# Kernel optimization log

Hardware: AMD Instinct MI355X
Metric: run time of the kernel (lower is better)

## Reference

```python
import jax, jax.numpy as jnp
import numpy as np

NUM_EXPERTS = 8
HIDDEN = 1024
INTER = 1024
TOKENS = 2048
TOPK = 2


def setup_inputs() -> dict:
    key = jax.random.key(0)
    ks = jax.random.split(key, 7)
    hidden_states = jax.random.normal(ks[0], (TOKENS, HIDDEN), dtype=jnp.float32)
    router_weights = jax.random.uniform(ks[1], (TOKENS, TOPK), dtype=jnp.float32)
    selected_experts = jax.random.randint(ks[2], (TOKENS, TOPK), 0, NUM_EXPERTS, dtype=jnp.int32)
    token_per_expert = jax.random.randint(ks[3], (NUM_EXPERTS,), 0, 512, dtype=jnp.int32)
    # torch Linear weight layout is [out, in]; chunked along out-dim into E experts.
    # gate/up: [E, INTER, HIDDEN]; down: [E, HIDDEN, INTER]
    scale_h = 1.0 / np.sqrt(HIDDEN)
    scale_i = 1.0 / np.sqrt(INTER)
    gate_w = jax.random.normal(ks[4], (NUM_EXPERTS, INTER, HIDDEN), dtype=jnp.float32) * scale_h
    up_w = jax.random.normal(ks[5], (NUM_EXPERTS, INTER, HIDDEN), dtype=jnp.float32) * scale_h
    down_w = jax.random.normal(ks[6], (NUM_EXPERTS, HIDDEN, INTER), dtype=jnp.float32) * scale_i
    return {
        "hidden_states": hidden_states,
        "router_weights": router_weights,
        "selected_experts": selected_experts,
        "token_per_expert": token_per_expert,
        "gate_w": gate_w,
        "up_w": up_w,
        "down_w": down_w,
    }


def reference(hidden_states, router_weights, selected_experts, token_per_expert, gate_w, up_w, down_w):
    # Math equivalent of permute -> grouped GEMM (gate/up SwiGLU, down) -> unpermute+weighted combine.
    # Each (token, k) pair is routed to expert selected_experts[t,k] and scaled by router_weights[t,k]
    # (cast to fp32 as in the original), then summed over k.
    # Grouped GEMM out = x @ W_e^T; we evaluate every expert densely over all tokens and
    # combine with a one-hot routing matrix (clean, fully vectorized reference).
    x = hidden_states  # [T, H]
    g = jnp.einsum('th,eih->eti', x, gate_w)          # [E, T, I]
    u = jnp.einsum('th,eih->eti', x, up_w)            # [E, T, I]
    h = jax.nn.silu(g) * u                            # [E, T, I]
    out_e = jnp.einsum('eti,ehi->eth', h, down_w)     # [E, T, H]
    # combine[t, e] = sum_k router_weights[t, k] * 1[selected_experts[t, k] == e]
    onehot = jax.nn.one_hot(selected_experts, NUM_EXPERTS, dtype=jnp.float32)  # [T, K, E]
    combine = jnp.einsum('tk,tke->te', router_weights.astype(jnp.float32), onehot)  # [T, E]
    y = jnp.einsum('te,eth->th', combine, out_e)      # [T, H]
    return y
```

## Files before the change

### kernel.cpp

```cpp
#include <hip/hip_runtime.h>
#include <hip/hip_bf16.h>

#define HID   1024
#define NEXP  8
#define NPAIR 4096
#define BMPAD 128
#define PERM_MAX (NPAIR + NEXP * BMPAD)
#define MT_MAX (PERM_MAX / 128)

typedef unsigned short u16;
typedef __attribute__((ext_vector_type(8))) short bf16x8;
typedef __attribute__((ext_vector_type(4))) float f32x4;
typedef __attribute__((ext_vector_type(4))) unsigned short us4;
typedef __attribute__((ext_vector_type(4))) unsigned int u32x4;

static __device__ __forceinline__ u16 f2bf(float f) {
  union { float f; unsigned u; } v; v.f = f;
  unsigned u = v.u;
  unsigned r = (u + 0x7fffu + ((u >> 16) & 1u)) >> 16;
  return (u16)r;
}

static __device__ __forceinline__ unsigned pk2(float a, float b) {
  __hip_bfloat162 h = __float22bfloat162_rn(make_float2(a, b));
  union { __hip_bfloat162 h; unsigned u; } c; c.h = h; return c.u;
}

static __device__ __forceinline__ void gload16(const void* g, void* l) {
  __builtin_amdgcn_global_load_lds(
      (const __attribute__((address_space(1))) unsigned int*)g,
      (__attribute__((address_space(3))) unsigned int*)l, 16, 0, 0);
}

static __device__ __forceinline__ f32x4 mfma_bf16(bf16x8 a, bf16x8 b, f32x4 c) {
  return __builtin_amdgcn_mfma_f32_16x16x32_bf16(a, b, c, 0, 0, 0);
}

__global__ __launch_bounds__(256) void k_prep(const float* __restrict__ x,
                                              u16* __restrict__ xb,
                                              float* __restrict__ out) {
  int i = blockIdx.x * 256 + threadIdx.x;
  int base = i * 8;
  f32x4 v0 = *(const f32x4*)(x + base);
  f32x4 v1 = *(const f32x4*)(x + base + 4);
  us4 a = { f2bf(v0[0]), f2bf(v0[1]), f2bf(v0[2]), f2bf(v0[3]) };
  us4 b = { f2bf(v1[0]), f2bf(v1[1]), f2bf(v1[2]), f2bf(v1[3]) };
  *(us4*)(xb + base)     = a;
  *(us4*)(xb + base + 4) = b;
  f32x4 z = {0.f, 0.f, 0.f, 0.f};
  *(f32x4*)(out + base)     = z;
  *(f32x4*)(out + base + 4) = z;
}

__global__ __launch_bounds__(256) void k_route(const int* __restrict__ sel,
                                               int* __restrict__ hdr,
                                               int* __restrict__ perm) {
  __shared__ int cnt[NEXP];
  __shared__ int cur[NEXP];
  int tid = threadIdx.x;
  if (tid < NEXP) cnt[tid] = 0;
  __syncthreads();
  for (int p = tid; p < NPAIR; p += 256) atomicAdd(&cnt[sel[p]], 1);
  __syncthreads();
  if (tid == 0) {
    int acc = 0;
    for (int e = 0; e < NEXP; e++) {
      hdr[e] = acc;
      cur[e] = acc;
      acc += (cnt[e] + 127) & ~127;
    }
    hdr[NEXP] = acc;
  }
  __syncthreads();
  for (int i = tid; i < PERM_MAX; i += 256) perm[i] = -1;
  __syncthreads();
  for (int p = tid; p < NPAIR; p += 256) {
    int e = sel[p];
    int slot = atomicAdd(&cur[e], 1);
    perm[slot] = p;
  }
}

__global__ __launch_bounds__(256) void k_gateup(const u16* __restrict__ xb,
                                                const float* __restrict__ gw,
                                                const float* __restrict__ uw,
                                                const int* __restrict__ hdr,
                                                const int* __restrict__ perm,
                                                u16* __restrict__ hbuf) {
  __shared__ __align__(16) u16 lA[2][128 * 64];
  __shared__ __align__(16) u16 lBg[2][64 * 64];
  __shared__ __align__(16) u16 lBu[2][64 * 64];

  const int tid = threadIdx.x, lane = tid & 63, wv = tid >> 6;
  const int n0 = blockIdx.x * 64, m0 = blockIdx.y * 128;
  if (m0 >= hdr[NEXP]) return;
  int e = 0;
  #pragma unroll
  for (int k = 1; k < NEXP; k++) if (m0 >= hdr[k]) e = k;

  const u16* srcA[4]; int dstAo[4];
  #pragma unroll
  for (int j = 0; j < 4; j++) {
    int rt = wv * 32 + j * 8 + (lane >> 3);
    int p = perm[m0 + rt];
    int tok = (p < 0) ? 0 : (p >> 1);
    int sw = (lane & 7) ^ (rt & 7);
    srcA[j] = xb + (size_t)tok * HID + sw * 8;
    dstAo[j] = (wv * 32 + j * 8) * 64;
  }
  const int br = wv * 16 + (lane >> 2);
  const int cb = (lane & 3) * 16;
  const size_t eb = (size_t)e * (1 << 20);
  const float* pG = gw + eb + (size_t)(n0 + br) * HID + cb;
  const float* pU = uw + eb + (size_t)(n0 + br) * HID + cb;
  const int bws0 = br * 64 + ((((lane & 3) * 2 + 0) ^ (br & 7)) * 8);
  const int bws1 = br * 64 + ((((lane & 3) * 2 + 1) ^ (br & 7)) * 8);

  const int wm = wv >> 1, wn = wv & 1;
  const int fr = lane & 15, fq = lane >> 4;

  f32x4 vg[4], vu[4];
  f32x4 accg[4][2], accu[4][2];
  #pragma unroll
  for (int a = 0; a < 4; a++)
    #pragma unroll
    for (int b = 0; b < 2; b++) {
      accg[a][b] = (f32x4){0.f, 0.f, 0.f, 0.f};
      accu[a][b] = (f32x4){0.f, 0.f, 0.f, 0.f};
    }

#define GU_ISSUE(B, K0) { const int k0_ = (K0);                                   \
    _Pragma("unroll") for (int j = 0; j < 4; j++)                                 \
      gload16(srcA[j] + k0_, &lA[B][dstAo[j]]);                                   \
    _Pragma("unroll") for (int i = 0; i < 4; i++) {                               \
      vg[i] = *(const f32x4*)(pG + k0_ + i * 4);                                  \
      vu[i] = *(const f32x4*)(pU + k0_ + i * 4);                                  \
    } }

#define GU_CVTW(B) {                                                              \
    u32x4 w0 = { pk2(vg[0][0], vg[0][1]), pk2(vg[0][2], vg[0][3]),                \
                 pk2(vg[1][0], vg[1][1]), pk2(vg[1][2], vg[1][3]) };              \
    *(u32x4*)&lBg[B][bws0] = w0;                                                  \
    u32x4 w1 = { pk2(vg[2][0], vg[2][1]), pk2(vg[2][2], vg[2][3]),                \
                 pk2(vg[3][0], vg[3][1]), pk2(vg[3][2], vg[3][3]) };              \
    *(u32x4*)&lBg[B][bws1] = w1;                                                  \
    u32x4 w2 = { pk2(vu[0][0], vu[0][1]), pk2(vu[0][2], vu[0][3]),                \
                 pk2(vu[1][0], vu[1][1]), pk2(vu[1][2], vu[1][3]) };              \
    *(u32x4*)&lBu[B][bws0] = w2;                                                  \
    u32x4 w3 = { pk2(vu[2][0], vu[2][1]), pk2(vu[2][2], vu[2][3]),                \
                 pk2(vu[3][0], vu[3][1]), pk2(vu[3][2], vu[3][3]) };              \
    *(u32x4*)&lBu[B][bws1] = w3; }

#define GU_COMP(B) {                                                              \
    _Pragma("unroll") for (int kk2 = 0; kk2 < 2; kk2++) {                         \
      bf16x8 af[4], bg[2], bu[2];                                                 \
      _Pragma("unroll") for (int m2 = 0; m2 < 4; m2++) {                          \
        int r = wm * 64 + m2 * 16 + fr, q = kk2 * 4 + fq;                         \
        af[m2] = *(const bf16x8*)&lA[B][r * 64 + (q ^ (r & 7)) * 8];              \
      }                                                                           \
      _Pragma("unroll") for (int n2 = 0; n2 < 2; n2++) {                          \
        int r = wn * 32 + n2 * 16 + fr, q = kk2 * 4 + fq;                         \
        bg[n2] = *(const bf16x8*)&lBg[B][r * 64 + (q ^ (r & 7)) * 8];             \
        bu[n2] = *(const bf16x8*)&lBu[B][r * 64 + (q ^ (r & 7)) * 8];             \
      }                                                                           \
      _Pragma("unroll") for (int m2 = 0; m2 < 4; m2++)                            \
        _Pragma("unroll") for (int n2 = 0; n2 < 2; n2++) {                        \
          accg[m2][n2] = mfma_bf16(af[m2], bg[n2], accg[m2][n2]);                 \
          accu[m2][n2] = mfma_bf16(af[m2], bu[n2], accu[m2][n2]);                 \
        }                                                                         \
    } }

  GU_ISSUE(0, 0);
  GU_CVTW(0);
  __syncthreads();
  for (int kk = 0; kk < 16; kk += 2) {
    GU_ISSUE(1, (kk + 1) * 64);
    GU_COMP(0);
    GU_CVTW(1);
    __syncthreads();
    if (kk + 2 < 16) { GU_ISSUE(0, (kk + 2) * 64); }
    GU_COMP(1);
    if (kk + 2 < 16) { GU_CVTW(0); }
    __syncthreads();
  }
#undef GU_ISSUE
#undef GU_CVTW
#undef GU_COMP

  #pragma unroll
  for (int m2 = 0; m2 < 4; m2++)
    #pragma unroll
    for (int n2 = 0; n2 < 2; n2++)
      #pragma unroll
      for (int q = 0; q < 4; q++) {
        int row = m0 + wm * 64 + m2 * 16 + fq * 4 + q;
        int col = n0 + wn * 32 + n2 * 16 + fr;
        float g = accg[m2][n2][q];
        float u = accu[m2][n2][q];
        float h = (g / (1.0f + __expf(-g))) * u;
        hbuf[(size_t)row * HID + col] = f2bf(h);
      }
}

__global__ __launch_bounds__(256) void k_down(const u16* __restrict__ hbuf,
                                              const float* __restrict__ dw,
                                              const int* __restrict__ hdr,
                                              const int* __restrict__ perm,
                                              const float* __restrict__ rw,
                                              float* __restrict__ out) {
  __shared__ __align__(16) u16 lA[2][128 * 64];
  __shared__ __align__(16) u16 lB[2][64 * 64];

  const int tid = threadIdx.x, lane = tid & 63, wv = tid >> 6;
  const int n0 = blockIdx.x * 64, m0 = blockIdx.y * 128;
  if (m0 >= hdr[NEXP]) return;
  int e = 0;
  #pragma unroll
  for (int k = 1; k < NEXP; k++) if (m0 >= hdr[k]) e = k;

  const u16* srcA[4]; int dstAo[4];
  #pragma unroll
  for (int j = 0; j < 4; j++) {
    int rt = wv * 32 + j * 8 + (lane >> 3);
    int sw = (lane & 7) ^ (rt & 7);
    srcA[j] = hbuf + (size_t)(m0 + rt) * HID + sw * 8;
    dstAo[j] = (wv * 32 + j * 8) * 64;
  }
  const int br = wv * 16 + (lane >> 2);
  const int cb = (lane & 3) * 16;
  const size_t eb = (size_t)e * (1 << 20);
  const float* pB = dw + eb + (size_t)(n0 + br) * HID + cb;
  const int bws0 = br * 64 + ((((lane & 3) * 2 + 0) ^ (br & 7)) * 8);
  const int bws1 = br * 64 + ((((lane & 3) * 2 + 1) ^ (br & 7)) * 8);

  const int wm = wv >> 1, wn = wv & 1;
  const int fr = lane & 15, fq = lane >> 4;

  f32x4 vb[4];
  f32x4 acc[4][2];
  #pragma unroll
  for (int a = 0; a < 4; a++)
    #pragma unroll
    for (int b = 0; b < 2; b++) acc[a][b] = (f32x4){0.f, 0.f, 0.f, 0.f};

#define DN_ISSUE(B, K0) { const int k0_ = (K0);                                   \
    _Pragma("unroll") for (int j = 0; j < 4; j++)                                 \
      gload16(srcA[j] + k0_, &lA[B][dstAo[j]]);                                   \
    _Pragma("unroll") for (int i = 0; i < 4; i++)                                 \
      vb[i] = *(const f32x4*)(pB + k0_ + i * 4); }

#define DN_CVTW(B) {                                                              \
    u32x4 w0 = { pk2(vb[0][0], vb[0][1]), pk2(vb[0][2], vb[0][3]),                \
                 pk2(vb[1][0], vb[1][1]), pk2(vb[1][2], vb[1][3]) };              \
    *(u32x4*)&lB[B][bws0] = w0;                                                   \
    u32x4 w1 = { pk2(vb[2][0], vb[2][1]), pk2(vb[2][2], vb[2][3]),                \
                 pk2(vb[3][0], vb[3][1]), pk2(vb[3][2], vb[3][3]) };              \
    *(u32x4*)&lB[B][bws1] = w1; }

#define DN_COMP(B) {                                                              \
    _Pragma("unroll") for (int kk2 = 0; kk2 < 2; kk2++) {                         \
      bf16x8 af[4], bf[2];                                                        \
      _Pragma("unroll") for (int m2 = 0; m2 < 4; m2++) {                          \
        int r = wm * 64 + m2 * 16 + fr, q = kk2 * 4 + fq;                         \
        af[m2] = *(const bf16x8*)&lA[B][r * 64 + (q ^ (r & 7)) * 8];              \
      }                                                                           \
      _Pragma("unroll") for (int n2 = 0; n2 < 2; n2++) {                          \
        int r = wn * 32 + n2 * 16 + fr, q = kk2 * 4 + fq;                         \
        bf[n2] = *(const bf16x8*)&lB[B][r * 64 + (q ^ (r & 7)) * 8];              \
      }                                                                           \
      _Pragma("unroll") for (int m2 = 0; m2 < 4; m2++)                            \
        _Pragma("unroll") for (int n2 = 0; n2 < 2; n2++)                          \
          acc[m2][n2] = mfma_bf16(af[m2], bf[n2], acc[m2][n2]);                   \
    } }

  DN_ISSUE(0, 0);
  DN_CVTW(0);
  __syncthreads();
  for (int kk = 0; kk < 16; kk += 2) {
    DN_ISSUE(1, (kk + 1) * 64);
    DN_COMP(0);
    DN_CVTW(1);
    __syncthreads();
    if (kk + 2 < 16) { DN_ISSUE(0, (kk + 2) * 64); }
    DN_COMP(1);
    if (kk + 2 < 16) { DN_CVTW(0); }
    __syncthreads();
  }
#undef DN_ISSUE
#undef DN_CVTW
#undef DN_COMP

  #pragma unroll
  for (int m2 = 0; m2 < 4; m2++)
    #pragma unroll
    for (int q = 0; q < 4; q++) {
      int row = m0 + wm * 64 + m2 * 16 + fq * 4 + q;
      int p = perm[row];
      if (p < 0) continue;
      int t = p >> 1;
      float w = rw[p];
      #pragma unroll
      for (int n2 = 0; n2 < 2; n2++) {
        int col = n0 + wn * 32 + n2 * 16 + fr;
        atomicAdd(&out[(size_t)t * HID + col], acc[m2][n2][q] * w);
      }
    }
}

extern "C" void kernel_launch(void* const* d_in, const int* in_sizes, int n_in,
                              void* d_out, int out_size, void* d_ws, size_t ws_size,
                              hipStream_t stream) {
  const float* x   = (const float*)d_in[0];
  const float* rw  = (const float*)d_in[1];
  const int*   sel = (const int*)d_in[2];
  const float* gw  = (const float*)d_in[4];
  const float* uw  = (const float*)d_in[5];
  const float* dw  = (const float*)d_in[6];
  float* out = (float*)d_out;

  char* ws = (char*)d_ws;
  int*  hdr  = (int*)ws;
  int*  perm = (int*)(ws + 1024);
  u16*  xb   = (u16*)(ws + (1 << 16));
  u16*  hbuf = xb + (2 << 20);

  k_prep <<<dim3(1024), dim3(256), 0, stream>>>(x, xb, out);
  k_route<<<dim3(1),    dim3(256), 0, stream>>>(sel, hdr, perm);
  k_gateup<<<dim3(16, MT_MAX), dim3(256), 0, stream>>>(xb, gw, uw, hdr, perm, hbuf);
  k_down  <<<dim3(16, MT_MAX), dim3(256), 0, stream>>>(hbuf, dw, hdr, perm, rw, out);
}
```

Measured before the change: 115.3 us.

## Load expert weights straight into MFMA registers, drop LDS staging for B

Each wave now loads its own fp32 weight rows from global memory and converts them to bf16 MFMA B fragments in registers, so the B tile no longer goes through LDS. Every wave covers all 128 token rows against its own 16 or 32 output columns. The down kernel widens its N tile to 128, which halves its grid, and both kernels use a 1D grid with a remapped tile order plus a launch-bounds occupancy hint. This removes the LDS writes and reads and the barrier pressure for weights, at the cost of more registers and less coalesced per-lane global loads.

```diff
diff --git a/kernel.cpp b/kernel.cpp
--- a/kernel.cpp
+++ b/kernel.cpp
@@ -12,7 +12,6 @@
 typedef __attribute__((ext_vector_type(8))) short bf16x8;
 typedef __attribute__((ext_vector_type(4))) float f32x4;
 typedef __attribute__((ext_vector_type(4))) unsigned short us4;
-typedef __attribute__((ext_vector_type(4))) unsigned int u32x4;
 
 static __device__ __forceinline__ u16 f2bf(float f) {
   union { float f; unsigned u; } v; v.f = f;
@@ -24,6 +23,13 @@
 static __device__ __forceinline__ unsigned pk2(float a, float b) {
   __hip_bfloat162 h = __float22bfloat162_rn(make_float2(a, b));
   union { __hip_bfloat162 h; unsigned u; } c; c.h = h; return c.u;
+}
+
+static __device__ __forceinline__ bf16x8 cvt8(f32x4 a, f32x4 b) {
+  union { unsigned u[4]; bf16x8 v; } r;
+  r.u[0] = pk2(a[0], a[1]); r.u[1] = pk2(a[2], a[3]);
+  r.u[2] = pk2(b[0], b[1]); r.u[3] = pk2(b[2], b[3]);
+  return r.v;
 }
 
 static __device__ __forceinline__ void gload16(const void* g, void* l) {
@@ -81,18 +87,20 @@
   }
 }
 
-__global__ __launch_bounds__(256) void k_gateup(const u16* __restrict__ xb,
-                                                const float* __restrict__ gw,
-                                                const float* __restrict__ uw,
-                                                const int* __restrict__ hdr,
-                                                const int* __restrict__ perm,
-                                                u16* __restrict__ hbuf) {
+__global__ __launch_bounds__(256, 3) void k_gateup(const u16* __restrict__ xb,
+                                                   const float* __restrict__ gw,
+                                                   const float* __restrict__ uw,
+                                                   const int* __restrict__ hdr,
+                                                   const int* __restrict__ perm,
+                                                   u16* __restrict__ hbuf) {
   __shared__ __align__(16) u16 lA[2][128 * 64];
-  __shared__ __align__(16) u16 lBg[2][64 * 64];
-  __shared__ __align__(16) u16 lBu[2][64 * 64];
 
   const int tid = threadIdx.x, lane = tid & 63, wv = tid >> 6;
-  const int n0 = blockIdx.x * 64, m0 = blockIdx.y * 128;
+  const int wgid = blockIdx.x;
+  const int slot = wgid >> 3;
+  const int nt = ((slot & 1) << 3) | (wgid & 7);
+  const int mt = slot >> 1;
+  const int n0 = nt * 64, m0 = mt * 128;
   if (m0 >= hdr[NEXP]) return;
   int e = 0;
   #pragma unroll
@@ -108,111 +116,94 @@
     srcA[j] = xb + (size_t)tok * HID + sw * 8;
     dstAo[j] = (wv * 32 + j * 8) * 64;
   }
-  const int br = wv * 16 + (lane >> 2);
-  const int cb = (lane & 3) * 16;
+
+  const int fr = lane & 15, fq = lane >> 4;
   const size_t eb = (size_t)e * (1 << 20);
-  const float* pG = gw + eb + (size_t)(n0 + br) * HID + cb;
-  const float* pU = uw + eb + (size_t)(n0 + br) * HID + cb;
-  const int bws0 = br * 64 + ((((lane & 3) * 2 + 0) ^ (br & 7)) * 8);
-  const int bws1 = br * 64 + ((((lane & 3) * 2 + 1) ^ (br & 7)) * 8);
-
-  const int wm = wv >> 1, wn = wv & 1;
-  const int fr = lane & 15, fq = lane >> 4;
-
-  f32x4 vg[4], vu[4];
-  f32x4 accg[4][2], accu[4][2];
-  #pragma unroll
-  for (int a = 0; a < 4; a++)
+  const int brow = n0 + wv * 16 + fr;
+  const float* pG = gw + eb + (size_t)brow * HID + fq * 8;
+  const float* pU = uw + eb + (size_t)brow * HID + fq * 8;
+
+  f32x4 ng[2][2], nu[2][2];
+  bf16x8 fg[2], fu[2];
+  f32x4 ag[8], au[8];
+  #pragma unroll
+  for (int i = 0; i < 8; i++) {
+    ag[i] = (f32x4){0.f, 0.f, 0.f, 0.f};
+    au[i] = (f32x4){0.f, 0.f, 0.f, 0.f};
+  }
+
+#define GU_GLA(B, K0) {                                                        \
+    _Pragma("unroll") for (int j = 0; j < 4; j++)                              \
+      gload16(srcA[j] + (K0), &lA[B][dstAo[j]]); }
+
+#define GU_LOADB(K0) {                                                         \
+    _Pragma("unroll") for (int kk2 = 0; kk2 < 2; kk2++) {                      \
+      ng[kk2][0] = *(const f32x4*)(pG + (K0) + kk2 * 32);                      \
+      ng[kk2][1] = *(const f32x4*)(pG + (K0) + kk2 * 32 + 4);                  \
+      nu[kk2][0] = *(const f32x4*)(pU + (K0) + kk2 * 32);                      \
+      nu[kk2][1] = *(const f32x4*)(pU + (K0) + kk2 * 32 + 4);                  \
+    } }
+
+#define GU_CVTB() {                                                            \
+    fg[0] = cvt8(ng[0][0], ng[0][1]); fg[1] = cvt8(ng[1][0], ng[1][1]);        \
+    fu[0] = cvt8(nu[0][0], nu[0][1]); fu[1] = cvt8(nu[1][0], nu[1][1]); }
+
+#define GU_COMP(B) {                                                           \
+    _Pragma("unroll") for (int kk2 = 0; kk2 < 2; kk2++) {                      \
+      _Pragma("unroll") for (int m2 = 0; m2 < 8; m2++) {                       \
+        int r = m2 * 16 + fr, q = kk2 * 4 + fq;                                \
+        bf16x8 af = *(const bf16x8*)&lA[B][r * 64 + (q ^ (r & 7)) * 8];        \
+        ag[m2] = mfma_bf16(af, fg[kk2], ag[m2]);                               \
+        au[m2] = mfma_bf16(af, fu[kk2], au[m2]);                               \
+      }                                                                        \
+    } }
+
+  GU_GLA(0, 0);
+  GU_LOADB(0);
+  __syncthreads();
+  GU_CVTB();
+  for (int kk = 0; kk < 16; kk += 2) {
+    GU_GLA(1, (kk + 1) * 64);
+    GU_LOADB((kk + 1) * 64);
+    GU_COMP(0);
+    __syncthreads();
+    GU_CVTB();
+    if (kk + 2 < 16) { GU_GLA(0, (kk + 2) * 64); GU_LOADB((kk + 2) * 64); }
+    GU_COMP(1);
+    __syncthreads();
+    if (kk + 2 < 16) GU_CVTB();
+  }
+#undef GU_GLA
+#undef GU_LOADB
+#undef GU_CVTB
+#undef GU_COMP
+
+  #pragma unroll
+  for (int m2 = 0; m2 < 8; m2++)
     #pragma unroll
-    for (int b = 0; b < 2; b++) {
-      accg[a][b] = (f32x4){0.f, 0.f, 0.f, 0.f};
-      accu[a][b] = (f32x4){0.f, 0.f, 0.f, 0.f};
+    for (int q = 0; q < 4; q++) {
+      int row = m0 + m2 * 16 + fq * 4 + q;
+      int col = n0 + wv * 16 + fr;
+      float g = ag[m2][q];
+      float u = au[m2][q];
+      float h = (g / (1.0f + __expf(-g))) * u;
+      hbuf[(size_t)row * HID + col] = f2bf(h);
     }
-
-#define GU_ISSUE(B, K0) { const int k0_ = (K0);                                   \
-    _Pragma("unroll") for (int j = 0; j < 4; j++)                                 \
-      gload16(srcA[j] + k0_, &lA[B][dstAo[j]]);                                   \
-    _Pragma("unroll") for (int i = 0; i < 4; i++) {                               \
-      vg[i] = *(const f32x4*)(pG + k0_ + i * 4);                                  \
-      vu[i] = *(const f32x4*)(pU + k0_ + i * 4);                                  \
-    } }
-
-#define GU_CVTW(B) {                                                              \
-    u32x4 w0 = { pk2(vg[0][0], vg[0][1]), pk2(vg[0][2], vg[0][3]),                \
-                 pk2(vg[1][0], vg[1][1]), pk2(vg[1][2], vg[1][3]) };              \
-    *(u32x4*)&lBg[B][bws0] = w0;                                                  \
-    u32x4 w1 = { pk2(vg[2][0], vg[2][1]), pk2(vg[2][2], vg[2][3]),                \
-                 pk2(vg[3][0], vg[3][1]), pk2(vg[3][2], vg[3][3]) };              \
-    *(u32x4*)&lBg[B][bws1] = w1;                                                  \
-    u32x4 w2 = { pk2(vu[0][0], vu[0][1]), pk2(vu[0][2], vu[0][3]),                \
-                 pk2(vu[1][0], vu[1][1]), pk2(vu[1][2], vu[1][3]) };              \
-    *(u32x4*)&lBu[B][bws0] = w2;                                                  \
-    u32x4 w3 = { pk2(vu[2][0], vu[2][1]), pk2(vu[2][2], vu[2][3]),                \
-                 pk2(vu[3][0], vu[3][1]), pk2(vu[3][2], vu[3][3]) };              \
-    *(u32x4*)&lBu[B][bws1] = w3; }
-
-#define GU_COMP(B) {                                                              \
-    _Pragma("unroll") for (int kk2 = 0; kk2 < 2; kk2++) {                         \
-      bf16x8 af[4], bg[2], bu[2];                                                 \
-      _Pragma("unroll") for (int m2 = 0; m2 < 4; m2++) {                          \
-        int r = wm * 64 + m2 * 16 + fr, q = kk2 * 4 + fq;                         \
-        af[m2] = *(const bf16x8*)&lA[B][r * 64 + (q ^ (r & 7)) * 8];              \
-      }                                                                           \
-      _Pragma("unroll") for (int n2 = 0; n2 < 2; n2++) {                          \
-        int r = wn * 32 + n2 * 16 + fr, q = kk2 * 4 + fq;                         \
-        bg[n2] = *(const bf16x8*)&lBg[B][r * 64 + (q ^ (r & 7)) * 8];             \
-        bu[n2] = *(const bf16x8*)&lBu[B][r * 64 + (q ^ (r & 7)) * 8];             \
-      }                                                                           \
-      _Pragma("unroll") for (int m2 = 0; m2 < 4; m2++)                            \
-        _Pragma("unroll") for (int n2 = 0; n2 < 2; n2++) {                        \
-          accg[m2][n2] = mfma_bf16(af[m2], bg[n2], accg[m2][n2]);                 \
-          accu[m2][n2] = mfma_bf16(af[m2], bu[n2], accu[m2][n2]);                 \
-        }                                                                         \
-    } }
-
-  GU_ISSUE(0, 0);
-  GU_CVTW(0);
-  __syncthreads();
-  for (int kk = 0; kk < 16; kk += 2) {
-    GU_ISSUE(1, (kk + 1) * 64);
-    GU_COMP(0);
-    GU_CVTW(1);
-    __syncthreads();
-    if (kk + 2 < 16) { GU_ISSUE(0, (kk + 2) * 64); }
-    GU_COMP(1);
-    if (kk + 2 < 16) { GU_CVTW(0); }
-    __syncthreads();
-  }
-#undef GU_ISSUE
-#undef GU_CVTW
-#undef GU_COMP
-
-  #pragma unroll
-  for (int m2 = 0; m2 < 4; m2++)
-    #pragma unroll
-    for (int n2 = 0; n2 < 2; n2++)
-      #pragma unroll
-      for (int q = 0; q < 4; q++) {
-        int row = m0 + wm * 64 + m2 * 16 + fq * 4 + q;
-        int col = n0 + wn * 32 + n2 * 16 + fr;
-        float g = accg[m2][n2][q];
-        float u = accu[m2][n2][q];
-        float h = (g / (1.0f + __expf(-g))) * u;
-        hbuf[(size_t)row * HID + col] = f2bf(h);
-      }
-}
-
-__global__ __launch_bounds__(256) void k_down(const u16* __restrict__ hbuf,
-                                              const float* __restrict__ dw,
-                                              const int* __restrict__ hdr,
-                                              const int* __restrict__ perm,
-                                              const float* __restrict__ rw,
-                                              float* __restrict__ out) {
+}
+
+__global__ __launch_bounds__(256, 3) void k_down(const u16* __restrict__ hbuf,
+                                                 const float* __restrict__ dw,
+                                                 const int* __restrict__ hdr,
+                                                 const int* __restrict__ perm,
+                                                 const float* __restrict__ rw,
+                                                 float* __restrict__ out) {
   __shared__ __align__(16) u16 lA[2][128 * 64];
-  __shared__ __align__(16) u16 lB[2][64 * 64];
 
   const int tid = threadIdx.x, lane = tid & 63, wv = tid >> 6;
-  const int n0 = blockIdx.x * 64, m0 = blockIdx.y * 128;
+  const int wgid = blockIdx.x;
+  const int nt = wgid & 7;
+  const int mt = wgid >> 3;
+  const int n0 = nt * 128, m0 = mt * 128;
   if (m0 >= hdr[NEXP]) return;
   int e = 0;
   #pragma unroll
@@ -226,82 +217,82 @@
     srcA[j] = hbuf + (size_t)(m0 + rt) * HID + sw * 8;
     dstAo[j] = (wv * 32 + j * 8) * 64;
   }
-  const int br = wv * 16 + (lane >> 2);
-  const int cb = (lane & 3) * 16;
+
+  const int fr = lane & 15, fq = lane >> 4;
   const size_t eb = (size_t)e * (1 << 20);
-  const float* pB = dw + eb + (size_t)(n0 + br) * HID + cb;
-  const int bws0 = br * 64 + ((((lane & 3) * 2 + 0) ^ (br & 7)) * 8);
-  const int bws1 = br * 64 + ((((lane & 3) * 2 + 1) ^ (br & 7)) * 8);
-
-  const int wm = wv >> 1, wn = wv & 1;
-  const int fr = lane & 15, fq = lane >> 4;
-
-  f32x4 vb[4];
-  f32x4 acc[4][2];
-  #pragma unroll
-  for (int a = 0; a < 4; a++)
+  const float* pB[2];
+  #pragma unroll
+  for (int n2 = 0; n2 < 2; n2++) {
+    int brow = n0 + wv * 32 + n2 * 16 + fr;
+    pB[n2] = dw + eb + (size_t)brow * HID + fq * 8;
+  }
+
+  f32x4 nb[2][2][2];
+  bf16x8 fb[2][2];
+  f32x4 acc[8][2];
+  #pragma unroll
+  for (int i = 0; i < 8; i++)
     #pragma unroll
-    for (int b = 0; b < 2; b++) acc[a][b] = (f32x4){0.f, 0.f, 0.f, 0.f};
-
-#define DN_ISSUE(B, K0) { const int k0_ = (K0);                                   \
-    _Pragma("unroll") for (int j = 0; j < 4; j++)                                 \
-      gload16(srcA[j] + k0_, &lA[B][dstAo[j]]);                                   \
-    _Pragma("unroll") for (int i = 0; i < 4; i++)                                 \
-      vb[i] = *(const f32x4*)(pB + k0_ + i * 4); }
-
-#define DN_CVTW(B) {                                                              \
-    u32x4 w0 = { pk2(vb[0][0], vb[0][1]), pk2(vb[0][2], vb[0][3]),                \
-                 pk2(vb[1][0], vb[1][1]), pk2(vb[1][2], vb[1][3]) };              \
-    *(u32x4*)&lB[B][bws0] = w0;                                                   \
-    u32x4 w1 = { pk2(vb[2][0], vb[2][1]), pk2(vb[2][2], vb[2][3]),                \
-                 pk2(vb[3][0], vb[3][1]), pk2(vb[3][2], vb[3][3]) };              \
-    *(u32x4*)&lB[B][bws1] = w1; }
-
-#define DN_COMP(B) {                                                              \
-    _Pragma("unroll") for (int kk2 = 0; kk2 < 2; kk2++) {                         \
-      bf16x8 af[4], bf[2];                                                        \
-      _Pragma("unroll") for (int m2 = 0; m2 < 4; m2++) {                          \
-        int r = wm * 64 + m2 * 16 + fr, q = kk2 * 4 + fq;                         \
-        af[m2] = *(const bf16x8*)&lA[B][r * 64 + (q ^ (r & 7)) * 8];              \
-      }                                                                           \
-      _Pragma("unroll") for (int n2 = 0; n2 < 2; n2++) {                          \
-        int r = wn * 32 + n2 * 16 + fr, q = kk2 * 4 + fq;                         \
-        bf[n2] = *(const bf16x8*)&lB[B][r * 64 + (q ^ (r & 7)) * 8];              \
-      }                                                                           \
-      _Pragma("unroll") for (int m2 = 0; m2 < 4; m2++)                            \
-        _Pragma("unroll") for (int n2 = 0; n2 < 2; n2++)                          \
-          acc[m2][n2] = mfma_bf16(af[m2], bf[n2], acc[m2][n2]);                   \
+    for (int j = 0; j < 2; j++) acc[i][j] = (f32x4){0.f, 0.f, 0.f, 0.f};
+
+#define DN_GLA(B, K0) {                                                        \
+    _Pragma("unroll") for (int j = 0; j < 4; j++)                              \
+      gload16(srcA[j] + (K0), &lA[B][dstAo[j]]); }
+
+#define DN_LOADB(K0) {                                                         \
+    _Pragma("unroll") for (int n2 = 0; n2 < 2; n2++)                           \
+      _Pragma("unroll") for (int kk2 = 0; kk2 < 2; kk2++) {                    \
+        nb[n2][kk2][0] = *(const f32x4*)(pB[n2] + (K0) + kk2 * 32);            \
+        nb[n2][kk2][1] = *(const f32x4*)(pB[n2] + (K0) + kk2 * 32 + 4);        \
+      } }
+
+#define DN_CVTB() {                                                            \
+    _Pragma("unroll") for (int n2 = 0; n2 < 2; n2++) {                         \
+      fb[n2][0] = cvt8(nb[n2][0][0], nb[n2][0][1]);                            \
+      fb[n2][1] = cvt8(nb[n2][1][0], nb[n2][1][1]); } }
+
+#define DN_COMP(B) {                                                           \
+    _Pragma("unroll") for (int kk2 = 0; kk2 < 2; kk2++) {                      \
+      _Pragma("unroll") for (int m2 = 0; m2 < 8; m2++) {                       \
+        int r = m2 * 16 + fr, q = kk2 * 4 + fq;                                \
+        bf16x8 af = *(const bf16x8*)&lA[B][r * 64 + (q ^ (r & 7)) * 8];        \
+        acc[m2][0] = mfma_bf16(af, fb[0][kk2], acc[m2][0]);                    \
+        acc[m2][1] = mfma_bf16(af, fb[1][kk2], acc[m2][1]);                    \
+      }                                                                        \
     } }
 
-  DN_ISSUE(0, 0);
-  DN_CVTW(0);
-  __syncthreads();
+  DN_GLA(0, 0);
+  DN_LOADB(0);
+  __syncthreads();
+  DN_CVTB();
   for (int kk = 0; kk < 16; kk += 2) {
-    DN_ISSUE(1, (kk + 1) * 64);
+    DN_GLA(1, (kk + 1) * 64);
+    DN_LOADB((kk + 1) * 64);
     DN_COMP(0);
-    DN_CVTW(1);
     __syncthreads();
-    if (kk + 2 < 16) { DN_ISSUE(0, (kk + 2) * 64); }
+    DN_CVTB();
+    if (kk + 2 < 16) { DN_GLA(0, (kk + 2) * 64); DN_LOADB((kk + 2) * 64); }
     DN_COMP(1);
-    if (kk + 2 < 16) { DN_CVTW(0); }
     __syncthreads();
-  }
-#undef DN_ISSUE
-#undef DN_CVTW
+    if (kk + 2 < 16) DN_CVTB();
+  }
+#undef DN_GLA
+#undef DN_LOADB
+#undef DN_CVTB
 #undef DN_COMP
 
   #pragma unroll
-  for (int m2 = 0; m2 < 4; m2++)
+  for (int m2 = 0; m2 < 8; m2++)
     #pragma unroll
     for (int q = 0; q < 4; q++) {
-      int row = m0 + wm * 64 + m2 * 16 + fq * 4 + q;
+      int row = m0 + m2 * 16 + fq * 4 + q;
       int p = perm[row];
       if (p < 0) continue;
       int t = p >> 1;
       float w = rw[p];
       #pragma unroll
       for (int n2 = 0; n2 < 2; n2++) {
-        int col = n0 + wn * 32 + n2 * 16 + fr;
+        int col = n0 + wv * 32 + n2 * 16 + fr;
         atomicAdd(&out[(size_t)t * HID + col], acc[m2][n2][q] * w);
       }
     }
@@ -326,6 +317,6 @@
 
   k_prep <<<dim3(1024), dim3(256), 0, stream>>>(x, xb, out);
   k_route<<<dim3(1),    dim3(256), 0, stream>>>(sel, hdr, perm);
-  k_gateup<<<dim3(16, MT_MAX), dim3(256), 0, stream>>>(xb, gw, uw, hdr, perm, hbuf);
-  k_down  <<<dim3(16, MT_MAX), dim3(256), 0, stream>>>(hbuf, dw, hdr, perm, rw, out);
-}
+  k_gateup<<<dim3(16 * MT_MAX), dim3(256), 0, stream>>>(xb, gw, uw, hdr, perm, hbuf);
+  k_down  <<<dim3(8 * MT_MAX),  dim3(256), 0, stream>>>(hbuf, dw, hdr, perm, rw, out);
+}
```

After: 135.7 us. 17.7% more time.

## Single-buffer B tiles and overlap prefetch with compute using lgkm-only barriers

Applied to the files above, without the earlier changes.

Both grouped-GEMM kernels now keep only the A tile double-buffered in LDS. The fp32 weight tile is held in registers and converted into a single LDS B buffer at the start of each k-step. The next A tile and the next weights are then issued before the barrier. `__syncthreads` is replaced by an inline-asm barrier that waits only on lgkmcnt, so global prefetches stay in flight during the MFMA compute. The goal is to hide memory latency and cut LDS use, which can raise occupancy. The catch is that correctness of the async LDS loads now depends on the compiler's vmcnt waits for the register weight loads, which are ordered after them.

```diff
diff --git a/kernel.cpp b/kernel.cpp
--- a/kernel.cpp
+++ b/kernel.cpp
@@ -13,6 +13,8 @@
 typedef __attribute__((ext_vector_type(4))) float f32x4;
 typedef __attribute__((ext_vector_type(4))) unsigned short us4;
 typedef __attribute__((ext_vector_type(4))) unsigned int u32x4;
+
+#define BAR() asm volatile("s_waitcnt lgkmcnt(0)\ns_barrier" ::: "memory")
 
 static __device__ __forceinline__ u16 f2bf(float f) {
   union { float f; unsigned u; } v; v.f = f;
@@ -88,8 +90,8 @@
                                                 const int* __restrict__ perm,
                                                 u16* __restrict__ hbuf) {
   __shared__ __align__(16) u16 lA[2][128 * 64];
-  __shared__ __align__(16) u16 lBg[2][64 * 64];
-  __shared__ __align__(16) u16 lBu[2][64 * 64];
+  __shared__ __align__(16) u16 lBg[64 * 64];
+  __shared__ __align__(16) u16 lBu[64 * 64];
 
   const int tid = threadIdx.x, lane = tid & 63, wv = tid >> 6;
   const int n0 = blockIdx.x * 64, m0 = blockIdx.y * 128;
@@ -129,61 +131,64 @@
       accu[a][b] = (f32x4){0.f, 0.f, 0.f, 0.f};
     }
 
-#define GU_ISSUE(B, K0) { const int k0_ = (K0);                                   \
-    _Pragma("unroll") for (int j = 0; j < 4; j++)                                 \
-      gload16(srcA[j] + k0_, &lA[B][dstAo[j]]);                                   \
-    _Pragma("unroll") for (int i = 0; i < 4; i++) {                               \
-      vg[i] = *(const f32x4*)(pG + k0_ + i * 4);                                  \
-      vu[i] = *(const f32x4*)(pU + k0_ + i * 4);                                  \
+#define GU_GLA(B, K0) {                                                        \
+    _Pragma("unroll") for (int j = 0; j < 4; j++)                              \
+      gload16(srcA[j] + (K0), &lA[B][dstAo[j]]); }
+
+#define GU_LOADB(K0) {                                                         \
+    _Pragma("unroll") for (int i = 0; i < 4; i++) {                            \
+      vg[i] = *(const f32x4*)(pG + (K0) + i * 4);                              \
+      vu[i] = *(const f32x4*)(pU + (K0) + i * 4);                              \
     } }
 
-#define GU_CVTW(B) {                                                              \
-    u32x4 w0 = { pk2(vg[0][0], vg[0][1]), pk2(vg[0][2], vg[0][3]),                \
-                 pk2(vg[1][0], vg[1][1]), pk2(vg[1][2], vg[1][3]) };              \
-    *(u32x4*)&lBg[B][bws0] = w0;                                                  \
-    u32x4 w1 = { pk2(vg[2][0], vg[2][1]), pk2(vg[2][2], vg[2][3]),                \
-                 pk2(vg[3][0], vg[3][1]), pk2(vg[3][2], vg[3][3]) };              \
-    *(u32x4*)&lBg[B][bws1] = w1;                                                  \
-    u32x4 w2 = { pk2(vu[0][0], vu[0][1]), pk2(vu[0][2], vu[0][3]),                \
-                 pk2(vu[1][0], vu[1][1]), pk2(vu[1][2], vu[1][3]) };              \
-    *(u32x4*)&lBu[B][bws0] = w2;                                                  \
-    u32x4 w3 = { pk2(vu[2][0], vu[2][1]), pk2(vu[2][2], vu[2][3]),                \
-                 pk2(vu[3][0], vu[3][1]), pk2(vu[3][2], vu[3][3]) };              \
-    *(u32x4*)&lBu[B][bws1] = w3; }
-
-#define GU_COMP(B) {                                                              \
-    _Pragma("unroll") for (int kk2 = 0; kk2 < 2; kk2++) {                         \
-      bf16x8 af[4], bg[2], bu[2];                                                 \
-      _Pragma("unroll") for (int m2 = 0; m2 < 4; m2++) {                          \
-        int r = wm * 64 + m2 * 16 + fr, q = kk2 * 4 + fq;                         \
-        af[m2] = *(const bf16x8*)&lA[B][r * 64 + (q ^ (r & 7)) * 8];              \
-      }                                                                           \
-      _Pragma("unroll") for (int n2 = 0; n2 < 2; n2++) {                          \
-        int r = wn * 32 + n2 * 16 + fr, q = kk2 * 4 + fq;                         \
-        bg[n2] = *(const bf16x8*)&lBg[B][r * 64 + (q ^ (r & 7)) * 8];             \
-        bu[n2] = *(const bf16x8*)&lBu[B][r * 64 + (q ^ (r & 7)) * 8];             \
-      }                                                                           \
-      _Pragma("unroll") for (int m2 = 0; m2 < 4; m2++)                            \
-        _Pragma("unroll") for (int n2 = 0; n2 < 2; n2++) {                        \
-          accg[m2][n2] = mfma_bf16(af[m2], bg[n2], accg[m2][n2]);                 \
-          accu[m2][n2] = mfma_bf16(af[m2], bu[n2], accu[m2][n2]);                 \
-        }                                                                         \
+#define GU_CVTW() {                                                            \
+    u32x4 w0 = { pk2(vg[0][0], vg[0][1]), pk2(vg[0][2], vg[0][3]),             \
+                 pk2(vg[1][0], vg[1][1]), pk2(vg[1][2], vg[1][3]) };           \
+    *(u32x4*)&lBg[bws0] = w0;                                                  \
+    u32x4 w1 = { pk2(vg[2][0], vg[2][1]), pk2(vg[2][2], vg[2][3]),             \
+                 pk2(vg[3][0], vg[3][1]), pk2(vg[3][2], vg[3][3]) };           \
+    *(u32x4*)&lBg[bws1] = w1;                                                  \
+    u32x4 w2 = { pk2(vu[0][0], vu[0][1]), pk2(vu[0][2], vu[0][3]),             \
+                 pk2(vu[1][0], vu[1][1]), pk2(vu[1][2], vu[1][3]) };           \
+    *(u32x4*)&lBu[bws0] = w2;                                                  \
+    u32x4 w3 = { pk2(vu[2][0], vu[2][1]), pk2(vu[2][2], vu[2][3]),             \
+                 pk2(vu[3][0], vu[3][1]), pk2(vu[3][2], vu[3][3]) };           \
+    *(u32x4*)&lBu[bws1] = w3; }
+
+#define GU_COMP(B) {                                                           \
+    _Pragma("unroll") for (int kk2 = 0; kk2 < 2; kk2++) {                      \
+      bf16x8 af[4], bg[2], bu[2];                                              \
+      _Pragma("unroll") for (int m2 = 0; m2 < 4; m2++) {                       \
+        int r = wm * 64 + m2 * 16 + fr, q = kk2 * 4 + fq;                      \
+        af[m2] = *(const bf16x8*)&lA[B][r * 64 + (q ^ (r & 7)) * 8];           \
+      }                                                                        \
+      _Pragma("unroll") for (int n2 = 0; n2 < 2; n2++) {                       \
+        int r = wn * 32 + n2 * 16 + fr, q = kk2 * 4 + fq;                      \
+        bg[n2] = *(const bf16x8*)&lBg[r * 64 + (q ^ (r & 7)) * 8];             \
+        bu[n2] = *(const bf16x8*)&lBu[r * 64 + (q ^ (r & 7)) * 8];             \
+      }                                                                        \
+      _Pragma("unroll") for (int m2 = 0; m2 < 4; m2++)                         \
+        _Pragma("unroll") for (int n2 = 0; n2 < 2; n2++) {                     \
+          accg[m2][n2] = mfma_bf16(af[m2], bg[n2], accg[m2][n2]);              \
+          accu[m2][n2] = mfma_bf16(af[m2], bu[n2], accu[m2][n2]);              \
+        }                                                                      \
     } }
 
-  GU_ISSUE(0, 0);
-  GU_CVTW(0);
-  __syncthreads();
-  for (int kk = 0; kk < 16; kk += 2) {
-    GU_ISSUE(1, (kk + 1) * 64);
-    GU_COMP(0);
-    GU_CVTW(1);
-    __syncthreads();
-    if (kk + 2 < 16) { GU_ISSUE(0, (kk + 2) * 64); }
-    GU_COMP(1);
-    if (kk + 2 < 16) { GU_CVTW(0); }
-    __syncthreads();
-  }
-#undef GU_ISSUE
+  GU_GLA(0, 0);
+  GU_LOADB(0);
+  for (int t = 0; t < 16; ++t) {
+    const int c = t & 1;
+    GU_CVTW();
+    if (t < 15) {
+      GU_GLA(c ^ 1, (t + 1) * 64);
+      GU_LOADB((t + 1) * 64);
+    }
+    BAR();
+    GU_COMP(c);
+    BAR();
+  }
+#undef GU_GLA
+#undef GU_LOADB
 #undef GU_CVTW
 #undef GU_COMP
 
@@ -209,7 +214,7 @@
                                               const float* __restrict__ rw,
                                               float* __restrict__ out) {
   __shared__ __align__(16) u16 lA[2][128 * 64];
-  __shared__ __align__(16) u16 lB[2][64 * 64];
+  __shared__ __align__(16) u16 lB[64 * 64];
 
   const int tid = threadIdx.x, lane = tid & 63, wv = tid >> 6;
   const int n0 = blockIdx.x * 64, m0 = blockIdx.y * 128;
@@ -243,50 +248,53 @@
     #pragma unroll
     for (int b = 0; b < 2; b++) acc[a][b] = (f32x4){0.f, 0.f, 0.f, 0.f};
 
-#define DN_ISSUE(B, K0) { const int k0_ = (K0);                                   \
-    _Pragma("unroll") for (int j = 0; j < 4; j++)                                 \
-      gload16(srcA[j] + k0_, &lA[B][dstAo[j]]);                                   \
-    _Pragma("unroll") for (int i = 0; i < 4; i++)                                 \
-      vb[i] = *(const f32x4*)(pB + k0_ + i * 4); }
-
-#define DN_CVTW(B) {                                                              \
-    u32x4 w0 = { pk2(vb[0][0], vb[0][1]), pk2(vb[0][2], vb[0][3]),                \
-                 pk2(vb[1][0], vb[1][1]), pk2(vb[1][2], vb[1][3]) };              \
-    *(u32x4*)&lB[B][bws0] = w0;                                                   \
-    u32x4 w1 = { pk2(vb[2][0], vb[2][1]), pk2(vb[2][2], vb[2][3]),                \
-                 pk2(vb[3][0], vb[3][1]), pk2(vb[3][2], vb[3][3]) };              \
-    *(u32x4*)&lB[B][bws1] = w1; }
-
-#define DN_COMP(B) {                                                              \
-    _Pragma("unroll") for (int kk2 = 0; kk2 < 2; kk2++) {                         \
-      bf16x8 af[4], bf[2];                                                        \
-      _Pragma("unroll") for (int m2 = 0; m2 < 4; m2++) {                          \
-        int r = wm * 64 + m2 * 16 + fr, q = kk2 * 4 + fq;                         \
-        af[m2] = *(const bf16x8*)&lA[B][r * 64 + (q ^ (r & 7)) * 8];              \
-      }                                                                           \
-      _Pragma("unroll") for (int n2 = 0; n2 < 2; n2++) {                          \
-        int r = wn * 32 + n2 * 16 + fr, q = kk2 * 4 + fq;                         \
-        bf[n2] = *(const bf16x8*)&lB[B][r * 64 + (q ^ (r & 7)) * 8];              \
-      }                                                                           \
-      _Pragma("unroll") for (int m2 = 0; m2 < 4; m2++)                            \
-        _Pragma("unroll") for (int n2 = 0; n2 < 2; n2++)                          \
-          acc[m2][n2] = mfma_bf16(af[m2], bf[n2], acc[m2][n2]);                   \
+#define DN_GLA(B, K0) {                                                        \
+    _Pragma("unroll") for (int j = 0; j < 4; j++)                              \
+      gload16(srcA[j] + (K0), &lA[B][dstAo[j]]); }
+
+#define DN_LOADB(K0) {                                                         \
+    _Pragma("unroll") for (int i = 0; i < 4; i++)                              \
+      vb[i] = *(const f32x4*)(pB + (K0) + i * 4); }
+
+#define DN_CVTW() {                                                            \
+    u32x4 w0 = { pk2(vb[0][0], vb[0][1]), pk2(vb[0][2], vb[0][3]),             \
+                 pk2(vb[1][0], vb[1][1]), pk2(vb[1][2], vb[1][3]) };           \
+    *(u32x4*)&lB[bws0] = w0;                                                   \
+    u32x4 w1 = { pk2(vb[2][0], vb[2][1]), pk2(vb[2][2], vb[2][3]),             \
+                 pk2(vb[3][0], vb[3][1]), pk2(vb[3][2], vb[3][3]) };           \
+    *(u32x4*)&lB[bws1] = w1; }
+
+#define DN_COMP(B) {                                                           \
+    _Pragma("unroll") for (int kk2 = 0; kk2 < 2; kk2++) {                      \
+      bf16x8 af[4], bf[2];                                                     \
+      _Pragma("unroll") for (int m2 = 0; m2 < 4; m2++) {                       \
+        int r = wm * 64 + m2 * 16 + fr, q = kk2 * 4 + fq;                      \
+        af[m2] = *(const bf16x8*)&lA[B][r * 64 + (q ^ (r & 7)) * 8];           \
+      }                                                                        \
+      _Pragma("unroll") for (int n2 = 0; n2 < 2; n2++) {                       \
+        int r = wn * 32 + n2 * 16 + fr, q = kk2 * 4 + fq;                      \
+        bf[n2] = *(const bf16x8*)&lB[r * 64 + (q ^ (r & 7)) * 8];              \
+      }                                                                        \
+      _Pragma("unroll") for (int m2 = 0; m2 < 4; m2++)                         \
+        _Pragma("unroll") for (int n2 = 0; n2 < 2; n2++)                       \
+          acc[m2][n2] = mfma_bf16(af[m2], bf[n2], acc[m2][n2]);                \
     } }
 
-  DN_ISSUE(0, 0);
-  DN_CVTW(0);
-  __syncthreads();
-  for (int kk = 0; kk < 16; kk += 2) {
-    DN_ISSUE(1, (kk + 1) * 64);
-    DN_COMP(0);
-    DN_CVTW(1);
-    __syncthreads();
-    if (kk + 2 < 16) { DN_ISSUE(0, (kk + 2) * 64); }
-    DN_COMP(1);
-    if (kk + 2 < 16) { DN_CVTW(0); }
-    __syncthreads();
-  }
-#undef DN_ISSUE
+  DN_GLA(0, 0);
+  DN_LOADB(0);
+  for (int t = 0; t < 16; ++t) {
+    const int c = t & 1;
+    DN_CVTW();
+    if (t < 15) {
+      DN_GLA(c ^ 1, (t + 1) * 64);
+      DN_LOADB((t + 1) * 64);
+    }
+    BAR();
+    DN_COMP(c);
+    BAR();
+  }
+#undef DN_GLA
+#undef DN_LOADB
 #undef DN_CVTW
 #undef DN_COMP
 
```

After: 111.6 us. -3.2%, faster.
